# Kernel tuning notes

Hardware: AMD Instinct MI355X
Metric: run time of the kernel (lower is better)

Reference implementation:

```python
import jax, jax.numpy as jnp
import numpy as np

K = 16  # kNN neighbors


def _knn(xb, k):
    # xb: [N, H] -> [N, k] nearest-neighbor indices (self excluded)
    sq = jnp.sum(xb * xb, axis=-1)
    d = sq[:, None] + sq[None, :] - 2.0 * (xb @ xb.T)  # squared distances [N, N]
    n = xb.shape[0]
    big = jnp.asarray(1e30, d.dtype)
    d = d + jnp.eye(n, dtype=d.dtype) * big  # mask self-loops
    _, idx = jax.lax.top_k(-d, k)
    return idx


def _edgeconv(h, W0, b0, W1, b1, k):
    # Dynamic kNN graph on current features + EdgeConv with 2-layer MLP, aggr='add'
    idx = jax.vmap(lambda xb: _knn(xb, k))(h)                 # [B, N, k]
    xj = jax.vmap(lambda xb, ib: xb[ib])(h, idx)              # [B, N, k, H] gather neighbors
    xi = jnp.broadcast_to(h[:, :, None, :], xj.shape)         # [B, N, k, H]
    m = jnp.concatenate([xi, xj - xi], axis=-1)               # [B, N, k, 2H]
    e = jax.nn.elu(m @ W0 + b0)
    e = jax.nn.elu(e @ W1 + b1)
    return jnp.sum(e, axis=2)                                 # 'add' aggregation over neighbors


def _forward(x, W_in0, b_in0, W_in1, b_in1, W_in2, b_in2,
             W_e0, b_e0, W_e1, b_e1,
             W_o0, b_o0, W_o1, b_o1, W_o2, b_o2):
    # input network (in_layers=3)
    h = jax.nn.elu(x @ W_in0 + b_in0)
    h = jax.nn.elu(h @ W_in1 + b_in1)
    h = jax.nn.elu(h @ W_in2 + b_in2)
    # agg_layers=2 blocks of dynamic-kNN EdgeConv
    for l in range(W_e0.shape[0]):
        h = _edgeconv(h, W_e0[l], b_e0[l], W_e1[l], b_e1[l], K)
    # global max pool over nodes of each graph (pool='max')
    g = jnp.max(h, axis=1)                                    # [B, H]
    # output network (out_layers=3)
    g = jax.nn.elu(g @ W_o0 + b_o0)
    g = jax.nn.elu(g @ W_o1 + b_o1)
    logits = g @ W_o2 + b_o2
    return jax.nn.log_softmax(logits, axis=1)


def setup_inputs() -> dict:
    key = jax.random.key(0)
    ks = jax.random.split(key, 8)
    B, N, F, H, C, A = 128, 512, 5, 64, 10, 2
    s = jnp.float32(0.1)

    def w(k, shape):
        return jax.random.normal(k, shape, jnp.float32) * s

    return {
        'x': jax.random.normal(ks[0], (B, N, F), jnp.float32),
        'W_in0': w(ks[1], (F, H)), 'b_in0': jnp.zeros((H,), jnp.float32),
        'W_in1': w(ks[2], (H, H)), 'b_in1': jnp.zeros((H,), jnp.float32),
        'W_in2': w(ks[3], (H, H)), 'b_in2': jnp.zeros((H,), jnp.float32),
        'W_e0': w(ks[4], (A, 2 * H, H)), 'b_e0': jnp.zeros((A, H), jnp.float32),
        'W_e1': w(ks[5], (A, H, H)), 'b_e1': jnp.zeros((A, H), jnp.float32),
        'W_o0': w(ks[6], (H, H)), 'b_o0': jnp.zeros((H,), jnp.float32),
        'W_o1': w(ks[7], (H, H)), 'b_o1': jnp.zeros((H,), jnp.float32),
        'W_o2': w(jax.random.fold_in(key, 99), (H, C)), 'b_o2': jnp.zeros((C,), jnp.float32),
    }


def reference(x, W_in0, b_in0, W_in1, b_in1, W_in2, b_in2,
              W_e0, b_e0, W_e1, b_e1,
              W_o0, b_o0, W_o1, b_o1, W_o2, b_o2):
    return _forward(x, W_in0, b_in0, W_in1, b_in1, W_in2, b_in2,
                    W_e0, b_e0, W_e1, b_e1,
                    W_o0, b_o0, W_o1, b_o1, W_o2, b_o2)
```

## Files before the change

kernel.cpp:

```cpp
#include <hip/hip_runtime.h>
#include <cmath>

typedef _Float16 f16;
typedef _Float16 f16x8 __attribute__((ext_vector_type(8)));
typedef float f32x4 __attribute__((ext_vector_type(4)));

#define B_ 128
#define N_ 512
#define H_ 64
#define K_ 16

__device__ __forceinline__ float elu_(float x) { return x > 0.f ? x : (__expf(x) - 1.f); }
__device__ __forceinline__ unsigned umin_(unsigned a, unsigned b) { return a < b ? a : b; }
__device__ __forceinline__ unsigned umax_(unsigned a, unsigned b) { return a > b ? a : b; }
__device__ __forceinline__ f32x4 mfma16(f16x8 a, f16x8 b, f32x4 c) {
    return __builtin_amdgcn_mfma_f32_16x16x32_f16(a, b, c, 0, 0, 0);
}
__device__ __forceinline__ f32x4 splat4(float v) { f32x4 r; r[0]=v; r[1]=v; r[2]=v; r[3]=v; return r; }
__device__ __forceinline__ unsigned mbcnt_(unsigned long long mask) {
    return __builtin_amdgcn_mbcnt_hi((unsigned)(mask >> 32),
           __builtin_amdgcn_mbcnt_lo((unsigned)mask, 0u));
}

__global__ __launch_bounds__(256) void mlp_kernel(const float* __restrict__ x,
        const float* __restrict__ W0, const float* __restrict__ b0,
        const float* __restrict__ W1, const float* __restrict__ b1,
        const float* __restrict__ W2, const float* __restrict__ b2,
        const float* __restrict__ We, const float* __restrict__ be,
        f16* __restrict__ hout, float* __restrict__ sqout,
        f16* __restrict__ Pout, f16* __restrict__ Qout)
{
    __shared__ f16 tile[4][16*72];
    const int lane = threadIdx.x & 63, wid = threadIdx.x >> 6;
    const int m = lane & 15, q = lane >> 4;
    const int rowbase = blockIdx.x*64 + wid*16;
    f16* tw = tile[wid];

    f16x8 af0, af1;
    {
        const float* xp = x + (size_t)(rowbase + m)*5;
        #pragma unroll
        for (int jj = 0; jj < 8; ++jj) { int k = q*8+jj; af0[jj] = (k < 5) ? (f16)xp[k] : (f16)0.f; }
    }
    f32x4 acc[4];
    #pragma unroll
    for (int t = 0; t < 4; ++t) {
        f16x8 bf;
        #pragma unroll
        for (int jj = 0; jj < 8; ++jj) { int k = q*8+jj; bf[jj] = (k < 5) ? (f16)W0[k*64 + t*16+m] : (f16)0.f; }
        acc[t] = splat4(b0[t*16+m]);
        acc[t] = mfma16(af0, bf, acc[t]);
    }
    #pragma unroll
    for (int t = 0; t < 4; ++t)
        #pragma unroll
        for (int r = 0; r < 4; ++r)
            tw[(q*4+r)*72 + t*16+m] = (f16)elu_(acc[t][r]);
    __syncthreads();
    af0 = *(const f16x8*)(tw + m*72 + q*8);
    af1 = *(const f16x8*)(tw + m*72 + q*8 + 32);
    __syncthreads();

    #pragma unroll
    for (int t = 0; t < 4; ++t) {
        f16x8 bfa, bfb;
        #pragma unroll
        for (int jj = 0; jj < 8; ++jj) {
            bfa[jj] = (f16)W1[(q*8+jj)*64 + t*16+m];
            bfb[jj] = (f16)W1[(q*8+jj+32)*64 + t*16+m];
        }
        acc[t] = splat4(b1[t*16+m]);
        acc[t] = mfma16(af0, bfa, acc[t]);
        acc[t] = mfma16(af1, bfb, acc[t]);
    }
    #pragma unroll
    for (int t = 0; t < 4; ++t)
        #pragma unroll
        for (int r = 0; r < 4; ++r)
            tw[(q*4+r)*72 + t*16+m] = (f16)elu_(acc[t][r]);
    __syncthreads();
    af0 = *(const f16x8*)(tw + m*72 + q*8);
    af1 = *(const f16x8*)(tw + m*72 + q*8 + 32);
    __syncthreads();

    #pragma unroll
    for (int t = 0; t < 4; ++t) {
        f16x8 bfa, bfb;
        #pragma unroll
        for (int jj = 0; jj < 8; ++jj) {
            bfa[jj] = (f16)W2[(q*8+jj)*64 + t*16+m];
            bfb[jj] = (f16)W2[(q*8+jj+32)*64 + t*16+m];
        }
        acc[t] = splat4(b2[t*16+m]);
        acc[t] = mfma16(af0, bfa, acc[t]);
        acc[t] = mfma16(af1, bfb, acc[t]);
    }
    float vv[4][4];
    float s[4] = {0.f,0.f,0.f,0.f};
    #pragma unroll
    for (int t = 0; t < 4; ++t)
        #pragma unroll
        for (int r = 0; r < 4; ++r) {
            float v = elu_(acc[t][r]);
            vv[t][r] = v;
            hout[(size_t)(rowbase + q*4 + r)*64 + t*16 + m] = (f16)v;
            s[r] += v*v;
        }
    #pragma unroll
    for (int off = 1; off <= 8; off <<= 1) {
        #pragma unroll
        for (int r = 0; r < 4; ++r) s[r] += __shfl_xor(s[r], off);
    }
    if (m == 0) {
        #pragma unroll
        for (int r = 0; r < 4; ++r) sqout[rowbase + q*4 + r] = s[r];
    }
    #pragma unroll
    for (int t = 0; t < 4; ++t)
        #pragma unroll
        for (int r = 0; r < 4; ++r)
            tw[(q*4+r)*72 + t*16+m] = (f16)vv[t][r];
    __syncthreads();
    af0 = *(const f16x8*)(tw + m*72 + q*8);
    af1 = *(const f16x8*)(tw + m*72 + q*8 + 32);

    f32x4 aP[4], aQ[4];
    #pragma unroll
    for (int t = 0; t < 4; ++t) { aP[t] = splat4(be[t*16+m]); aQ[t] = splat4(0.f); }
    #pragma unroll
    for (int cc = 0; cc < 2; ++cc) {
        const f16x8 afc = cc ? af1 : af0;
        #pragma unroll
        for (int t = 0; t < 4; ++t) {
            f16x8 bp, bq;
            #pragma unroll
            for (int jj = 0; jj < 8; ++jj) {
                float wa = We[(q*8+jj+32*cc)*64 + t*16+m];
                float wb = We[(q*8+jj+32*cc+64)*64 + t*16+m];
                bq[jj] = (f16)wb; bp[jj] = (f16)(wa - wb);
            }
            aP[t] = mfma16(afc, bp, aP[t]);
            aQ[t] = mfma16(afc, bq, aQ[t]);
        }
    }
    #pragma unroll
    for (int t = 0; t < 4; ++t)
        #pragma unroll
        for (int r = 0; r < 4; ++r) {
            Pout[(size_t)(rowbase + q*4 + r)*64 + t*16 + m] = (f16)aP[t][r];
            Qout[(size_t)(rowbase + q*4 + r)*64 + t*16 + m] = (f16)aQ[t][r];
        }
}

#define KIDX(row, col) ((row)*512 + ((col) ^ ((row) << 1)))

template<bool DOPQ>
__global__ __launch_bounds__(512, 8) void knn_kernel(const f16* __restrict__ hin,
        const float* __restrict__ sq, int* __restrict__ idxout,
        const float* __restrict__ We, const float* __restrict__ be,
        f16* __restrict__ Pout, f16* __restrict__ Qout)
{
    __shared__ unsigned keys[16*512];
    const int lane = threadIdx.x & 63;
    const int wid  = threadIdx.x >> 6;
    const int m = lane & 15, q = lane >> 4;
    const int b  = blockIdx.x >> 5;
    const int rt = blockIdx.x & 31;
    const int rowbase = rt*16;
    const f16* hb = hin + (size_t)b*N_*H_;
    const float* sqb = sq + b*N_;

    f16x8 af0, af1;
    {
        const f16* Ap = hb + (size_t)(rowbase + m)*64 + q*8;
        af0 = *(const f16x8*)Ap;
        af1 = *(const f16x8*)(Ap + 32);
    }
    #pragma unroll
    for (int ct = wid; ct < 32; ct += 8) {
        const int colbase = ct*16;
        const f16* Bp = hb + (size_t)(colbase + m)*64 + q*8;
        f16x8 bf0 = *(const f16x8*)Bp;
        f16x8 bf1 = *(const f16x8*)(Bp + 32);
        f32x4 acc = splat4(0.f);
        acc = mfma16(af0, bf0, acc);
        acc = mfma16(af1, bf1, acc);
        const float sc = sqb[colbase + m];
        #pragma unroll
        for (int r = 0; r < 4; ++r) {
            float d = fmaf(-2.f, acc[r], sc);
            unsigned u = __float_as_uint(d);
            u ^= (0x80000000u | (unsigned)((int)u >> 31));
            unsigned key = (u & 0xFFFFFE00u) | (unsigned)(colbase + m);
            const int rowin = q*4 + r;
            if (colbase + m == rowbase + rowin) key = 0xFFFFFFFFu;
            keys[KIDX(rowin, colbase + m)] = key;
        }
    }

    if (DOPQ) {
        const int t = wid & 3;
        f32x4 acc = (wid < 4) ? splat4(be[t*16+m]) : splat4(0.f);
        #pragma unroll
        for (int cc = 0; cc < 2; ++cc) {
            const f16x8 afc = cc ? af1 : af0;
            f16x8 bb;
            if (wid < 4) {
                #pragma unroll
                for (int jj = 0; jj < 8; ++jj) {
                    float wa = We[(q*8+jj+32*cc)*64 + t*16+m];
                    float wb = We[(q*8+jj+32*cc+64)*64 + t*16+m];
                    bb[jj] = (f16)(wa - wb);
                }
            } else {
                #pragma unroll
                for (int jj = 0; jj < 8; ++jj)
                    bb[jj] = (f16)We[(q*8+jj+32*cc+64)*64 + t*16+m];
            }
            acc = mfma16(afc, bb, acc);
        }
        f16* outp = (wid < 4) ? Pout : Qout;
        #pragma unroll
        for (int r = 0; r < 4; ++r)
            outp[((size_t)b*N_ + rowbase + q*4 + r)*64 + t*16 + m] = (f16)acc[r];
    }
    __syncthreads();

    unsigned kk[2][8];
    #pragma unroll
    for (int rr = 0; rr < 2; ++rr) {
        const int ri = wid*2 + rr;
        *(uint4*)&kk[rr][0] = *(const uint4*)(keys + ri*512 + lane*4);
        *(uint4*)&kk[rr][4] = *(const uint4*)(keys + ri*512 + 256 + lane*4);
    }
    unsigned* scr = keys + wid*2*512;

    unsigned v[2];
    #pragma unroll
    for (int rr = 0; rr < 2; ++rr) {
        unsigned mn = kk[rr][0];
        #pragma unroll
        for (int s2 = 1; s2 < 8; ++s2) mn = umin_(mn, kk[rr][s2]);
        v[rr] = mn;
    }
    unsigned T[2] = {0u,0u};
    #pragma unroll
    for (int bit = 31; bit >= 9; --bit) {
        #pragma unroll
        for (int rr = 0; rr < 2; ++rr) {
            unsigned cand = T[rr] | (1u << bit);
            int c = __popcll(__ballot(v[rr] < cand));
            T[rr] = (c < 16) ? cand : T[rr];
        }
    }
    T[0] |= 511u; T[1] |= 511u;

    unsigned cnt[2];
    #pragma unroll
    for (int rr = 0; rr < 2; ++rr) {
        unsigned c = 0;
        #pragma unroll
        for (int s2 = 0; s2 < 8; ++s2) {
            const bool p = kk[rr][s2] <= T[rr];
            unsigned long long bal = __ballot(p);
            unsigned pos = c + mbcnt_(bal);
            if (p && pos < 64u) scr[rr*64 + pos] = kk[rr][s2];
            c += (unsigned)__popcll(bal);
        }
        cnt[rr] = c;
    }

    #pragma unroll
    for (int rr = 0; rr < 2; ++rr) {
        const unsigned cc_ = umin_(cnt[rr], 64u);
        bool act = lane < (int)cc_;
        unsigned mv = act ? scr[rr*64 + lane] : 0u;
        const int e = (int)cc_ - 16;
        for (int it = 0; it < e; ++it) {
            unsigned mx = mv;
            #pragma unroll
            for (int off = 1; off <= 32; off <<= 1) mx = umax_(mx, __shfl_xor(mx, off));
            if (mv == mx) { act = false; mv = 0u; }
        }
        const int ri = wid*2 + rr;
        int* outp = idxout + ((size_t)b*N_ + rowbase + ri)*K_;
        unsigned long long bal = __ballot(act);
        unsigned rank = mbcnt_(bal);
        if (act) outp[rank] = (int)(mv & 511u);
    }
}

__global__ __launch_bounds__(256, 5) void edge_kernel(const f16* __restrict__ P,
        const f16* __restrict__ Q, const int* __restrict__ idx,
        const float* __restrict__ W1, const float* __restrict__ b1,
        f16* __restrict__ out, float* __restrict__ sqout)
{
    const int lane = threadIdx.x & 63;
    const int wid  = threadIdx.x >> 6;
    const int m = lane & 15, q = lane >> 4;

    f16x8 bf[2][4];
    #pragma unroll
    for (int cc = 0; cc < 2; ++cc)
        #pragma unroll
        for (int t = 0; t < 4; ++t)
            #pragma unroll
            for (int jj = 0; jj < 8; ++jj)
                bf[cc][t][jj] = (f16)W1[(q*8 + jj + 32*cc)*64 + t*16 + m];
    float bcol[4];
    #pragma unroll
    for (int t = 0; t < 4; ++t) bcol[t] = b1[t*16 + m];

    const int node0 = blockIdx.x*32 + wid*8;
    for (int i = 0; i < 8; ++i) {
        const int r0 = node0 + i;
        const int j = idx[(size_t)r0*K_ + m];
        const int qrow = (r0 & ~(N_-1)) + j;
        f16x8 af[2];
        #pragma unroll
        for (int cc = 0; cc < 2; ++cc) {
            const int c0 = q*8 + 32*cc;
            f16x8 pv = *(const f16x8*)(P + (size_t)r0*64 + c0);
            f16x8 qv = *(const f16x8*)(Q + (size_t)qrow*64 + c0);
            #pragma unroll
            for (int jj = 0; jj < 8; ++jj)
                af[cc][jj] = (f16)elu_((float)pv[jj] + (float)qv[jj]);
        }
        f32x4 acc[4];
        #pragma unroll
        for (int t = 0; t < 4; ++t) acc[t] = splat4(bcol[t]);
        #pragma unroll
        for (int cc = 0; cc < 2; ++cc)
            #pragma unroll
            for (int t = 0; t < 4; ++t) acc[t] = mfma16(af[cc], bf[cc][t], acc[t]);
        float ssum = 0.f;
        #pragma unroll
        for (int t = 0; t < 4; ++t) {
            float s = elu_(acc[t][0]) + elu_(acc[t][1]) + elu_(acc[t][2]) + elu_(acc[t][3]);
            s += __shfl_xor(s, 16);
            s += __shfl_xor(s, 32);
            if (lane < 16) out[(size_t)r0*64 + t*16 + lane] = (f16)s;
            ssum += s*s;
        }
        #pragma unroll
        for (int off = 1; off <= 8; off <<= 1) ssum += __shfl_xor(ssum, off);
        if (lane == 0) sqout[r0] = ssum;
    }
}

__global__ __launch_bounds__(256) void final_kernel(const f16* __restrict__ hin,
        const float* __restrict__ Wo0, const float* __restrict__ bo0,
        const float* __restrict__ Wo1, const float* __restrict__ bo1,
        const float* __restrict__ Wo2, const float* __restrict__ bo2,
        float* __restrict__ out)
{
    __shared__ float smax[32][64];
    __shared__ float g0[64], g1[64], g2[64], part[4][64], lg[10];
    const int t = threadIdx.x;
    const int b = blockIdx.x;
    const int cg = t & 7, rg = t >> 3;

    float mx[8];
    #pragma unroll
    for (int e = 0; e < 8; ++e) mx[e] = -3.0e38f;
    #pragma unroll
    for (int i = 0; i < 16; ++i) {
        const int row = rg + i*32;
        f16x8 vv = *(const f16x8*)(hin + ((size_t)b*N_ + row)*64 + cg*8);
        #pragma unroll
        for (int e = 0; e < 8; ++e) mx[e] = fmaxf(mx[e], (float)vv[e]);
    }
    #pragma unroll
    for (int e = 0; e < 8; ++e) smax[rg][cg*8 + e] = mx[e];
    __syncthreads();
    for (int s = 16; s >= 1; s >>= 1) {
        if (rg < s) {
            #pragma unroll
            for (int e = 0; e < 8; ++e)
                smax[rg][cg*8+e] = fmaxf(smax[rg][cg*8+e], smax[rg+s][cg*8+e]);
        }
        __syncthreads();
    }
    if (t < 64) g0[t] = smax[0][t];
    __syncthreads();

    const int j = t & 63, p = t >> 6;
    {
        float a = 0.f;
        #pragma unroll
        for (int c = 0; c < 16; ++c) a += g0[p*16 + c]*Wo0[(p*16 + c)*64 + j];
        part[p][j] = a;
    }
    __syncthreads();
    if (t < 64) g1[t] = elu_(part[0][t] + part[1][t] + part[2][t] + part[3][t] + bo0[t]);
    __syncthreads();
    {
        float a = 0.f;
        #pragma unroll
        for (int c = 0; c < 16; ++c) a += g1[p*16 + c]*Wo1[(p*16 + c)*64 + j];
        part[p][j] = a;
    }
    __syncthreads();
    if (t < 64) g2[t] = elu_(part[0][t] + part[1][t] + part[2][t] + part[3][t] + bo1[t]);
    __syncthreads();
    if (t < 10) { float a = bo2[t]; for (int c = 0; c < 64; ++c) a += g2[c]*Wo2[c*10 + t]; lg[t] = a; }
    __syncthreads();
    if (t == 0) {
        float mxl = lg[0];
        for (int i = 1; i < 10; ++i) mxl = fmaxf(mxl, lg[i]);
        float s = 0.f;
        for (int i = 0; i < 10; ++i) s += expf(lg[i] - mxl);
        const float lse = mxl + logf(s);
        for (int i = 0; i < 10; ++i) out[b*10 + i] = lg[i] - lse;
    }
}

extern "C" void kernel_launch(void* const* d_in, const int* in_sizes, int n_in,
                              void* d_out, int out_size, void* d_ws, size_t ws_size,
                              hipStream_t stream) {
    const float* x     = (const float*)d_in[0];
    const float* W_in0 = (const float*)d_in[1];
    const float* b_in0 = (const float*)d_in[2];
    const float* W_in1 = (const float*)d_in[3];
    const float* b_in1 = (const float*)d_in[4];
    const float* W_in2 = (const float*)d_in[5];
    const float* b_in2 = (const float*)d_in[6];
    const float* W_e0  = (const float*)d_in[7];
    const float* b_e0  = (const float*)d_in[8];
    const float* W_e1  = (const float*)d_in[9];
    const float* b_e1  = (const float*)d_in[10];
    const float* Wo0   = (const float*)d_in[11];
    const float* bo0   = (const float*)d_in[12];
    const float* Wo1   = (const float*)d_in[13];
    const float* bo1   = (const float*)d_in[14];
    const float* Wo2   = (const float*)d_in[15];
    const float* bo2   = (const float*)d_in[16];

    char* ws = (char*)d_ws;
    f16*   hA   = (f16*)(ws);
    f16*   hB   = (f16*)(ws + 8388608);
    f16*   Pb   = (f16*)(ws + 16777216);
    f16*   Qb   = (f16*)(ws + 25165824);
    int*   idxb = (int*)(ws + 33554432);
    float* sqb  = (float*)(ws + 37748736);

    mlp_kernel<<<1024, 256, 0, stream>>>(x, W_in0, b_in0, W_in1, b_in1, W_in2, b_in2,
                                         W_e0, b_e0, hA, sqb, Pb, Qb);
    knn_kernel<false><<<4096, 512, 0, stream>>>(hA, sqb, idxb, nullptr, nullptr, nullptr, nullptr);
    edge_kernel<<<2048, 256, 0, stream>>>(Pb, Qb, idxb, W_e1, b_e1, hB, sqb);
    knn_kernel<true><<<4096, 512, 0, stream>>>(hB, sqb, idxb, W_e0 + 8192, b_e0 + 64, Pb, Qb);
    edge_kernel<<<2048, 256, 0, stream>>>(Pb, Qb, idxb, W_e1 + 4096, b_e1 + 64, hA, sqb);

    final_kernel<<<128, 256, 0, stream>>>(hA, Wo0, bo0, Wo1, bo1, Wo2, bo2, (float*)d_out);
}
```

Baseline: 301.3 us.

## Restructure kNN key build, move self-masking to selection, use half-precision ELU

The kNN kernel now hoists all B-fragment and squared-norm loads ahead of the MFMA loop, uses precomputed swizzled LDS offsets, and no longer masks the diagonal while building keys. Instead, the threshold search keeps 17 candidates and the self index is dropped during final selection. The top-k selection now runs before the optional P/Q projection, so that projection work can overlap with the memory-bound phases. In the edge kernel, the first ELU is computed in packed fp16 with hexp instead of per-element fp32 expf, which lowers precision on the activation.

```diff
diff --git a/kernel.cpp b/kernel.cpp
--- a/kernel.cpp
+++ b/kernel.cpp
@@ -1,4 +1,5 @@
 #include <hip/hip_runtime.h>
+#include <hip/hip_fp16.h>
 #include <cmath>
 
 typedef _Float16 f16;
@@ -20,6 +21,20 @@
 __device__ __forceinline__ unsigned mbcnt_(unsigned long long mask) {
     return __builtin_amdgcn_mbcnt_hi((unsigned)(mask >> 32),
            __builtin_amdgcn_mbcnt_lo((unsigned)mask, 0u));
+}
+__device__ __forceinline__ f16 hexp_(f16 x) {
+    __half h = *(__half*)&x; h = hexp(h); return *(f16*)&h;
+}
+__device__ __forceinline__ f16x8 elu8h_(f16x8 x) {
+    f16x8 z; f16x8 one;
+    #pragma unroll
+    for (int i = 0; i < 8; ++i) { z[i] = (f16)0.f; one[i] = (f16)1.f; }
+    f16x8 mx = __builtin_elementwise_max(x, z);
+    f16x8 mn = __builtin_elementwise_min(x, z);
+    f16x8 e;
+    #pragma unroll
+    for (int i = 0; i < 8; ++i) e[i] = hexp_(mn[i]);
+    return mx + e - one;
 }
 
 __global__ __launch_bounds__(256) void mlp_kernel(const float* __restrict__ x,
@@ -151,8 +166,6 @@
             Qout[(size_t)(rowbase + q*4 + r)*64 + t*16 + m] = (f16)aQ[t][r];
         }
 }
-
-#define KIDX(row, col) ((row)*512 + ((col) ^ ((row) << 1)))
 
 template<bool DOPQ>
 __global__ __launch_bounds__(512, 8) void knn_kernel(const f16* __restrict__ hin,
@@ -176,26 +189,101 @@
         af0 = *(const f16x8*)Ap;
         af1 = *(const f16x8*)(Ap + 32);
     }
-    #pragma unroll
-    for (int ct = wid; ct < 32; ct += 8) {
-        const int colbase = ct*16;
-        const f16* Bp = hb + (size_t)(colbase + m)*64 + q*8;
-        f16x8 bf0 = *(const f16x8*)Bp;
-        f16x8 bf1 = *(const f16x8*)(Bp + 32);
+    const int colb0 = wid*16;
+    f16x8 bf0[4], bf1[4];
+    float sc[4];
+    #pragma unroll
+    for (int cti = 0; cti < 4; ++cti) {
+        const f16* Bp = hb + (size_t)(colb0 + cti*128 + m)*64 + q*8;
+        bf0[cti] = *(const f16x8*)Bp;
+        bf1[cti] = *(const f16x8*)(Bp + 32);
+        sc[cti] = sqb[colb0 + cti*128 + m];
+    }
+    int base_r[4];
+    #pragma unroll
+    for (int r = 0; r < 4; ++r) {
+        const int row = q*4 + r;
+        base_r[r] = row*512 + ((colb0 + m) ^ (row << 1));
+    }
+    #pragma unroll
+    for (int cti = 0; cti < 4; ++cti) {
         f32x4 acc = splat4(0.f);
-        acc = mfma16(af0, bf0, acc);
-        acc = mfma16(af1, bf1, acc);
-        const float sc = sqb[colbase + m];
+        acc = mfma16(af0, bf0[cti], acc);
+        acc = mfma16(af1, bf1[cti], acc);
         #pragma unroll
         for (int r = 0; r < 4; ++r) {
-            float d = fmaf(-2.f, acc[r], sc);
+            float d = fmaf(-2.f, acc[r], sc[cti]);
             unsigned u = __float_as_uint(d);
             u ^= (0x80000000u | (unsigned)((int)u >> 31));
-            unsigned key = (u & 0xFFFFFE00u) | (unsigned)(colbase + m);
-            const int rowin = q*4 + r;
-            if (colbase + m == rowbase + rowin) key = 0xFFFFFFFFu;
-            keys[KIDX(rowin, colbase + m)] = key;
-        }
+            unsigned key = (u & 0xFFFFFE00u) | (unsigned)(colb0 + cti*128 + m);
+            keys[base_r[r] + cti*128] = key;
+        }
+    }
+    __syncthreads();
+
+    unsigned kk[2][8];
+    #pragma unroll
+    for (int rr = 0; rr < 2; ++rr) {
+        const int ri = wid*2 + rr;
+        *(uint4*)&kk[rr][0] = *(const uint4*)(keys + ri*512 + lane*4);
+        *(uint4*)&kk[rr][4] = *(const uint4*)(keys + ri*512 + 256 + lane*4);
+    }
+    unsigned* scr = keys + wid*2*512;
+
+    unsigned v[2];
+    #pragma unroll
+    for (int rr = 0; rr < 2; ++rr) {
+        unsigned mn = kk[rr][0];
+        #pragma unroll
+        for (int s2 = 1; s2 < 8; ++s2) mn = umin_(mn, kk[rr][s2]);
+        v[rr] = mn;
+    }
+    unsigned T[2] = {0u,0u};
+    #pragma unroll
+    for (int bit = 31; bit >= 9; --bit) {
+        #pragma unroll
+        for (int rr = 0; rr < 2; ++rr) {
+            unsigned cand = T[rr] | (1u << bit);
+            int c = __popcll(__ballot(v[rr] < cand));
+            T[rr] = (c < 17) ? cand : T[rr];
+        }
+    }
+    T[0] |= 511u; T[1] |= 511u;
+
+    unsigned cnt[2];
+    #pragma unroll
+    for (int rr = 0; rr < 2; ++rr) {
+        unsigned c = 0;
+        #pragma unroll
+        for (int s2 = 0; s2 < 8; ++s2) {
+            const bool p = kk[rr][s2] <= T[rr];
+            unsigned long long bal = __ballot(p);
+            unsigned pos = c + mbcnt_(bal);
+            if (p && pos < 64u) scr[rr*64 + pos] = kk[rr][s2];
+            c += (unsigned)__popcll(bal);
+        }
+        cnt[rr] = c;
+    }
+
+    #pragma unroll
+    for (int rr = 0; rr < 2; ++rr) {
+        const unsigned cc_ = umin_(cnt[rr], 64u);
+        const int ri = wid*2 + rr;
+        const unsigned rowglob = (unsigned)(rowbase + ri);
+        bool act = lane < (int)cc_;
+        unsigned mv = act ? scr[rr*64 + lane] : 0u;
+        if (act && (mv & 511u) == rowglob) { act = false; mv = 0u; }
+        const int e = __popcll(__ballot(act)) - 16;
+        for (int it = 0; it < e; ++it) {
+            unsigned mx = mv;
+            #pragma unroll
+            for (int off = 1; off <= 32; off <<= 1) mx = umax_(mx, __shfl_xor(mx, off));
+            if (act && mv == mx) { act = false; mv = 0u; }
+        }
+        int* outp = idxout + ((size_t)b*N_ + rowglob)*K_;
+        unsigned long long bal = __ballot(act);
+        unsigned rank = mbcnt_(bal);
+        if (act) outp[rank] = (int)(mv & 511u);
     }
 
     if (DOPQ) {
@@ -224,70 +312,6 @@
         for (int r = 0; r < 4; ++r)
             outp[((size_t)b*N_ + rowbase + q*4 + r)*64 + t*16 + m] = (f16)acc[r];
     }
-    __syncthreads();
-
-    unsigned kk[2][8];
-    #pragma unroll
-    for (int rr = 0; rr < 2; ++rr) {
-        const int ri = wid*2 + rr;
-        *(uint4*)&kk[rr][0] = *(const uint4*)(keys + ri*512 + lane*4);
-        *(uint4*)&kk[rr][4] = *(const uint4*)(keys + ri*512 + 256 + lane*4);
-    }
-    unsigned* scr = keys + wid*2*512;
-
-    unsigned v[2];
-    #pragma unroll
-    for (int rr = 0; rr < 2; ++rr) {
-        unsigned mn = kk[rr][0];
-        #pragma unroll
-        for (int s2 = 1; s2 < 8; ++s2) mn = umin_(mn, kk[rr][s2]);
-        v[rr] = mn;
-    }
-    unsigned T[2] = {0u,0u};
-    #pragma unroll
-    for (int bit = 31; bit >= 9; --bit) {
-        #pragma unroll
-        for (int rr = 0; rr < 2; ++rr) {
-            unsigned cand = T[rr] | (1u << bit);
-            int c = __popcll(__ballot(v[rr] < cand));
-            T[rr] = (c < 16) ? cand : T[rr];
-        }
-    }
-    T[0] |= 511u; T[1] |= 511u;
-
-    unsigned cnt[2];
-    #pragma unroll
-    for (int rr = 0; rr < 2; ++rr) {
-        unsigned c = 0;
-        #pragma unroll
-        for (int s2 = 0; s2 < 8; ++s2) {
-            const bool p = kk[rr][s2] <= T[rr];
-            unsigned long long bal = __ballot(p);
-            unsigned pos = c + mbcnt_(bal);
-            if (p && pos < 64u) scr[rr*64 + pos] = kk[rr][s2];
-            c += (unsigned)__popcll(bal);
-        }
-        cnt[rr] = c;
-    }
-
-    #pragma unroll
-    for (int rr = 0; rr < 2; ++rr) {
-        const unsigned cc_ = umin_(cnt[rr], 64u);
-        bool act = lane < (int)cc_;
-        unsigned mv = act ? scr[rr*64 + lane] : 0u;
-        const int e = (int)cc_ - 16;
-        for (int it = 0; it < e; ++it) {
-            unsigned mx = mv;
-            #pragma unroll
-            for (int off = 1; off <= 32; off <<= 1) mx = umax_(mx, __shfl_xor(mx, off));
-            if (mv == mx) { act = false; mv = 0u; }
-        }
-        const int ri = wid*2 + rr;
-        int* outp = idxout + ((size_t)b*N_ + rowbase + ri)*K_;
-        unsigned long long bal = __ballot(act);
-        unsigned rank = mbcnt_(bal);
-        if (act) outp[rank] = (int)(mv & 511u);
-    }
 }
 
 __global__ __launch_bounds__(256, 5) void edge_kernel(const f16* __restrict__ P,
@@ -322,9 +346,7 @@
             const int c0 = q*8 + 32*cc;
             f16x8 pv = *(const f16x8*)(P + (size_t)r0*64 + c0);
             f16x8 qv = *(const f16x8*)(Q + (size_t)qrow*64 + c0);
-            #pragma unroll
-            for (int jj = 0; jj < 8; ++jj)
-                af[cc][jj] = (f16)elu_((float)pv[jj] + (float)qv[jj]);
+            af[cc] = elu8h_(pv + qv);
         }
         f32x4 acc[4];
         #pragma unroll
```

Result: no change. 295.6 us (-1.9%).
